# Performance work log

Hardware: AMD Instinct MI355X
Metric: run time of the kernel (lower is better)

The kernel has to match this reference:

```python
import jax, jax.numpy as jnp
import numpy as np

N, E, B = 20000, 160000, 1000
D_IN, HID, HEADS, CTX, EDIM, L = 7, 64, 4, 3, 5, 4


def _ln(x, g, b):
    mu = x.mean(-1, keepdims=True)
    v = ((x - mu) ** 2).mean(-1, keepdims=True)
    return (x - mu) / jnp.sqrt(v + 1e-5) * g + b


def _seg_softmax(a, seg, n):
    m = jax.ops.segment_max(a, seg, num_segments=n)
    e = jnp.exp(a - m[seg])
    s = jax.ops.segment_sum(e, seg, num_segments=n)
    return e / (s[seg] + 1e-16)


def _forward(x, edge_index, edge_attr, context, batch, role, side, formation, alignment, frame_t,
             emb_W, emb_b, role_tab, side_tab, ctx_W, ctx_b, form_tab, align_tab, temp_tab,
             gat_Wl, gat_bl, gat_Wr, gat_br, gat_We, gat_att, gat_bias,
             ln_g, ln_b, sp_W1, sp_b1, sp_W2, sp_b2, sp_Wg, sp_bg, fn_g, fn_b):
    src, dst = edge_index[0], edge_index[1]
    h = jax.nn.relu(x @ emb_W + emb_b)                      # [N, HID]
    h = h + role_tab[role]
    s_emb = side_tab[side]                                   # [N, HID//2], zero-padded to HID
    h = h + jnp.pad(s_emb, ((0, 0), (0, HID - HID // 2)))
    t_idx = jnp.clip((frame_t[0] * 99).astype(jnp.int32), 0, 99)
    h = h + temp_tab[t_idx]
    c = jax.nn.relu(context @ ctx_W + ctx_b)                 # [B, HID]
    c = c + form_tab[formation] + align_tab[alignment]
    h = h + c[batch]
    # PyG GATv2Conv adds self-loops (fill_value='mean' for edge_attr)
    in_cnt = jax.ops.segment_sum(jnp.ones((E,), h.dtype), dst, num_segments=N)
    loop_attr = jax.ops.segment_sum(edge_attr, dst, num_segments=N) / jnp.maximum(in_cnt, 1.0)[:, None]
    srcA = jnp.concatenate([src, jnp.arange(N, dtype=src.dtype)])
    dstA = jnp.concatenate([dst, jnp.arange(N, dtype=dst.dtype)])
    eaA = jnp.concatenate([edge_attr, loop_attr], axis=0)    # [E+N, EDIM]
    EA = E + N
    for i in range(L):
        h_res = h
        xl = (h @ gat_Wl[i] + gat_bl[i]).reshape(N, HEADS, HID)
        xr = (h @ gat_Wr[i] + gat_br[i]).reshape(N, HEADS, HID)
        e = (eaA @ gat_We[i]).reshape(EA, HEADS, HID)
        msg = jax.nn.leaky_relu(xl[srcA] + xr[dstA] + e, 0.2)  # [EA, H, C]
        alpha = jnp.einsum('ehc,hc->eh', msg, gat_att[i])
        alpha = _seg_softmax(alpha, dstA, N)
        agg = jax.ops.segment_sum(xl[srcA] * alpha[:, :, None], dstA, num_segments=N)
        h = agg.mean(axis=1) + gat_bias[i]                   # concat=False -> mean over heads
        h = jax.nn.relu(h)                                   # dropout is identity in eval
        h = _ln(h + h_res, ln_g[i], ln_b[i])
    # Social pooling: gather -> MLP -> gate -> scatter-mean by src
    pair = jnp.concatenate([h[src], h[dst]], axis=-1)        # [E, 2*HID]
    inter = jax.nn.relu(pair @ sp_W1 + sp_b1) @ sp_W2 + sp_b2
    gated = inter * jax.nn.sigmoid(inter @ sp_Wg + sp_bg)
    cnt = jax.ops.segment_sum(jnp.ones((E,), h.dtype), src, num_segments=N)
    pooled = jax.ops.segment_sum(gated, src, num_segments=N) / jnp.maximum(cnt, 1.0)[:, None]
    h = _ln(h + pooled, fn_g, fn_b)
    return h


def setup_inputs():
    key = jax.random.key(0)
    ks = jax.random.split(key, 32)
    p = lambda k, shp: jax.random.normal(k, shp, jnp.float32) * 0.05
    return dict(
        x=jax.random.normal(ks[0], (N, D_IN), jnp.float32),
        edge_index=jax.random.randint(ks[1], (2, E), 0, N),
        edge_attr=jax.random.normal(ks[2], (E, EDIM), jnp.float32),
        context=jax.random.normal(ks[3], (B, CTX), jnp.float32),
        batch=jax.random.randint(ks[4], (N,), 0, B),
        role=jax.random.randint(ks[5], (N,), 0, 5),
        side=jax.random.randint(ks[6], (N,), 0, 3),
        formation=jax.random.randint(ks[7], (B,), 0, 8),
        alignment=jax.random.randint(ks[8], (B,), 0, 10),
        frame_t=jax.random.uniform(ks[9], (1,), jnp.float32),
        emb_W=p(ks[10], (D_IN, HID)), emb_b=p(ks[11], (HID,)),
        role_tab=p(ks[12], (5, HID)), side_tab=p(ks[13], (3, HID // 2)),
        ctx_W=p(ks[14], (CTX, HID)), ctx_b=p(ks[15], (HID,)),
        form_tab=p(ks[16], (8, HID)), align_tab=p(ks[17], (10, HID)),
        temp_tab=p(ks[18], (100, HID)),
        gat_Wl=p(ks[19], (L, HID, HEADS * HID)), gat_bl=p(ks[20], (L, HEADS * HID)),
        gat_Wr=p(ks[21], (L, HID, HEADS * HID)), gat_br=p(ks[22], (L, HEADS * HID)),
        gat_We=p(ks[23], (L, EDIM, HEADS * HID)),
        gat_att=p(ks[24], (L, HEADS, HID)), gat_bias=p(ks[25], (L, HID)),
        ln_g=jnp.ones((L, HID), jnp.float32), ln_b=jnp.zeros((L, HID), jnp.float32),
        sp_W1=p(ks[26], (2 * HID, HID)), sp_b1=p(ks[27], (HID,)),
        sp_W2=p(ks[28], (HID, HID)), sp_b2=p(ks[29], (HID,)),
        sp_Wg=p(ks[30], (HID, HID)), sp_bg=p(ks[31], (HID,)),
        fn_g=jnp.ones((HID,), jnp.float32), fn_b=jnp.zeros((HID,), jnp.float32),
    )


def reference(x, edge_index, edge_attr, context, batch, role, side, formation, alignment, frame_t,
              emb_W, emb_b, role_tab, side_tab, ctx_W, ctx_b, form_tab, align_tab, temp_tab,
              gat_Wl, gat_bl, gat_Wr, gat_br, gat_We, gat_att, gat_bias,
              ln_g, ln_b, sp_W1, sp_b1, sp_W2, sp_b2, sp_Wg, sp_bg, fn_g, fn_b):
    return _forward(x, edge_index, edge_attr, context, batch, role, side, formation, alignment, frame_t,
                    emb_W, emb_b, role_tab, side_tab, ctx_W, ctx_b, form_tab, align_tab, temp_tab,
                    gat_Wl, gat_bl, gat_Wr, gat_br, gat_We, gat_att, gat_bias,
                    ln_g, ln_b, sp_W1, sp_b1, sp_W2, sp_b2, sp_Wg, sp_bg, fn_g, fn_b)
```

## Files before the change

kernel.cpp:

```cpp
#include <hip/hip_runtime.h>
#include <math.h>

constexpr int N = 20000, E = 160000, Bb = 1000;
constexpr int DIN = 7, HID = 64, HEADS = 4, CTXD = 3, EDIM = 5, NL = 4;
constexpr int HH = HEADS * HID;

__device__ __forceinline__ float wredsum(float v) {
#pragma unroll
  for (int o = 32; o; o >>= 1) v += __shfl_xor(v, o, 64);
  return v;
}

__global__ void k_node_init(const float* __restrict__ x, const float* __restrict__ emb_W,
                            const float* __restrict__ emb_b, const int* __restrict__ role,
                            const float* __restrict__ role_tab, const int* __restrict__ side,
                            const float* __restrict__ side_tab, const float* __restrict__ frame_t,
                            const float* __restrict__ temp_tab, const int* __restrict__ batch,
                            const float* __restrict__ ctx, const float* __restrict__ ctx_W,
                            const float* __restrict__ ctx_b, const float* __restrict__ form_tab,
                            const float* __restrict__ align_tab, const int* __restrict__ form,
                            const int* __restrict__ alig, float* __restrict__ h) {
  int t = blockIdx.x * blockDim.x + threadIdx.x;
  if (t >= N * HID) return;
  int n = t >> 6, j = t & 63;
  float a = emb_b[j];
#pragma unroll
  for (int k = 0; k < DIN; ++k) a += x[n * DIN + k] * emb_W[k * HID + j];
  a = fmaxf(a, 0.f);
  a += role_tab[role[n] * HID + j];
  if (j < 32) a += side_tab[side[n] * 32 + j];
  int ti = (int)(frame_t[0] * 99.f);
  ti = ti < 0 ? 0 : (ti > 99 ? 99 : ti);
  a += temp_tab[ti * HID + j];
  int b = batch[n];
  float c = ctx_b[j];
#pragma unroll
  for (int k = 0; k < CTXD; ++k) c += ctx[b * CTXD + k] * ctx_W[k * HID + j];
  c = fmaxf(c, 0.f);
  c += form_tab[form[b] * HID + j] + align_tab[alig[b] * HID + j];
  h[t] = a + c;
}

__global__ void k_count(const int* __restrict__ ei, int* __restrict__ deg_dst,
                        int* __restrict__ deg_src) {
  int e = blockIdx.x * blockDim.x + threadIdx.x;
  if (e >= E) return;
  atomicAdd(&deg_src[ei[e]], 1);
  atomicAdd(&deg_dst[ei[E + e]], 1);
}

__global__ void k_fuse(const float* __restrict__ W2, const float* __restrict__ Wg,
                       const float* __restrict__ b2, const float* __restrict__ bg,
                       float* __restrict__ W2g, float* __restrict__ bg2) {
  int t = blockIdx.x * 256 + threadIdx.x;
  if (t < HID * HID) {
    int i = t >> 6, j = t & 63;
    float a = 0.f;
#pragma unroll
    for (int k = 0; k < HID; ++k) a += W2[i * HID + k] * Wg[k * HID + j];
    W2g[t] = a;
  }
  if (t < HID) {
    float a = bg[t];
#pragma unroll
    for (int k = 0; k < HID; ++k) a += b2[k] * Wg[k * HID + t];
    bg2[t] = a;
  }
}

__global__ void k_scan2(const int* __restrict__ degA, int* __restrict__ rowA,
                        int* __restrict__ curA, const int* __restrict__ degB,
                        int* __restrict__ rowB, int* __restrict__ curB, int n) {
  __shared__ int wsum[16];
  __shared__ int carry;
  int t = threadIdx.x, wid = t >> 6, lane = t & 63;
  for (int pass = 0; pass < 2; ++pass) {
    const int* deg = pass ? degB : degA;
    int* row = pass ? rowB : rowA;
    int* cur = pass ? curB : curA;
    if (t == 0) carry = 0;
    __syncthreads();
    for (int base = 0; base < n; base += 1024) {
      int v = (base + t < n) ? deg[base + t] : 0;
      int s = v;
#pragma unroll
      for (int off = 1; off < 64; off <<= 1) {
        int x = __shfl_up(s, off, 64);
        if (lane >= off) s += x;
      }
      if (lane == 63) wsum[wid] = s;
      __syncthreads();
      if (wid == 0) {
        int ws = (lane < 16) ? wsum[lane] : 0;
#pragma unroll
        for (int off = 1; off < 16; off <<= 1) {
          int x = __shfl_up(ws, off, 64);
          if (lane >= off) ws += x;
        }
        if (lane < 16) wsum[lane] = ws;
      }
      __syncthreads();
      int wexcl = (wid == 0) ? 0 : wsum[wid - 1];
      int r = carry + wexcl + (s - v);
      if (base + t < n) {
        row[base + t] = r;
        cur[base + t] = r;
      }
      __syncthreads();
      if (t == 0) carry += wsum[15];
      __syncthreads();
    }
  }
}

__global__ void k_scatter(const int* __restrict__ ei, int* __restrict__ cur_dst,
                          int* __restrict__ cur_src, int* __restrict__ eid_dst,
                          int* __restrict__ esrc_dst, int* __restrict__ esrc_srt,
                          int* __restrict__ edst_srt) {
  int e = blockIdx.x * blockDim.x + threadIdx.x;
  if (e >= E) return;
  int s = ei[e], d = ei[E + e];
  int ps = atomicAdd(&cur_src[s], 1);
  esrc_srt[ps] = s;
  edst_srt[ps] = d;
  int pd = atomicAdd(&cur_dst[d], 1);
  eid_dst[pd] = e;
  esrc_dst[pd] = s;
}

__global__ void k_loop_attr(const int* __restrict__ row_dst, const int* __restrict__ deg_dst,
                            const int* __restrict__ eid_dst, const float* __restrict__ ea,
                            float* __restrict__ la) {
  int n = blockIdx.x * blockDim.x + threadIdx.x;
  if (n >= N) return;
  int beg = row_dst[n], cnt = deg_dst[n];
  float s[EDIM] = {0.f, 0.f, 0.f, 0.f, 0.f};
  for (int j = 0; j < cnt; ++j) {
    int e = eid_dst[beg + j];
#pragma unroll
    for (int k = 0; k < EDIM; ++k) s[k] += ea[(size_t)e * EDIM + k];
  }
  float inv = 1.f / fmaxf((float)cnt, 1.f);
#pragma unroll
  for (int k = 0; k < EDIM; ++k) la[n * EDIM + k] = s[k] * inv;
}

__global__ __launch_bounds__(256) void k_xlxr(const float* __restrict__ h,
                                              const float* __restrict__ Wl,
                                              const float* __restrict__ bl,
                                              const float* __restrict__ Wr,
                                              const float* __restrict__ br,
                                              float* __restrict__ xl, float* __restrict__ xr) {
  constexpr int NB = 16;
  __shared__ float hs[NB][HID];
  int n0 = blockIdx.x * NB;
  for (int idx = threadIdx.x; idx < NB * HID; idx += 256) {
    int r = idx >> 6, c = idx & 63;
    hs[r][c] = h[(n0 + r) * HID + c];
  }
  __syncthreads();
  int t = threadIdx.x;
  float wl[HID], wr[HID];
#pragma unroll
  for (int k = 0; k < HID; ++k) {
    wl[k] = Wl[k * HH + t];
    wr[k] = Wr[k * HH + t];
  }
  float blv = bl[t], brv = br[t];
#pragma unroll 4
  for (int r = 0; r < NB; ++r) {
    float al = blv, ar = brv;
#pragma unroll
    for (int k = 0; k < HID; ++k) {
      float hv = hs[r][k];
      al += hv * wl[k];
      ar += hv * wr[k];
    }
    xl[(size_t)(n0 + r) * HH + t] = al;
    xr[(size_t)(n0 + r) * HH + t] = ar;
  }
}

__global__ __launch_bounds__(256) void k_gat(
    const float* __restrict__ xl, const float* __restrict__ xr, const float* __restrict__ ea,
    const float* __restrict__ la, const int* __restrict__ row_dst,
    const int* __restrict__ deg_dst, const int* __restrict__ eid_dst,
    const int* __restrict__ esrc_dst, const float* __restrict__ We,
    const float* __restrict__ att, const float* __restrict__ biasL,
    const float* __restrict__ lng, const float* __restrict__ lnb, float* __restrict__ h) {
  __shared__ float heads[HEADS][HID];
  int n = blockIdx.x;
  int w = threadIdx.x >> 6, lane = threadIdx.x & 63;
  int g = lane >> 4, q = lane & 15, c4 = q * 4;
  float4 xr4 = *(const float4*)(xr + (size_t)n * HH + w * HID + c4);
  float4 att4 = *(const float4*)(att + w * HID + c4);
  float4 we4[EDIM];
#pragma unroll
  for (int k = 0; k < EDIM; ++k) we4[k] = *(const float4*)(We + k * HH + w * HID + c4);
  int beg = row_dst[n], cnt = deg_dst[n];
  int tot = cnt + 1;
  float mg = -INFINITY, sg = 0.f;
  float ax = 0.f, ay = 0.f, az = 0.f, aw2 = 0.f;
  int srcn_p;
  const float* eap_p;
  if (g == 0 || g >= tot) {
    srcn_p = n;
    eap_p = la + (size_t)n * EDIM;
  } else {
    int pos = beg + g - 1;
    srcn_p = esrc_dst[pos];
    eap_p = ea + (size_t)eid_dst[pos] * EDIM;
  }
  for (int j = 0; j * 4 < tot; ++j) {
    int idx = j * 4 + g;
    int srcn = srcn_p;
    const float* eap = eap_p;
    int idx2 = idx + 4;
    if (idx2 >= tot) {
      srcn_p = n;
      eap_p = la + (size_t)n * EDIM;
    } else {
      int pos = beg + idx2 - 1;
      srcn_p = esrc_dst[pos];
      eap_p = ea + (size_t)eid_dst[pos] * EDIM;
    }
    if (idx < tot) {
      float4 ep;
      ep.x = ep.y = ep.z = ep.w = 0.f;
#pragma unroll
      for (int k = 0; k < EDIM; ++k) {
        float ev = eap[k];
        ep.x += ev * we4[k].x;
        ep.y += ev * we4[k].y;
        ep.z += ev * we4[k].z;
        ep.w += ev * we4[k].w;
      }
      float4 xl4 = *(const float4*)(xl + (size_t)srcn * HH + w * HID + c4);
      float v0 = xl4.x + xr4.x + ep.x;
      float v1 = xl4.y + xr4.y + ep.y;
      float v2 = xl4.z + xr4.z + ep.z;
      float v3 = xl4.w + xr4.w + ep.w;
      v0 = v0 > 0.f ? v0 : 0.2f * v0;
      v1 = v1 > 0.f ? v1 : 0.2f * v1;
      v2 = v2 > 0.f ? v2 : 0.2f * v2;
      v3 = v3 > 0.f ? v3 : 0.2f * v3;
      float dot = v0 * att4.x + v1 * att4.y + v2 * att4.z + v3 * att4.w;
#pragma unroll
      for (int o = 1; o < 16; o <<= 1) dot += __shfl_xor(dot, o, 64);
      float nm = fmaxf(mg, dot);
      float sc = __expf(mg - nm);
      float pp = __expf(dot - nm);
      sg = sg * sc + pp;
      ax = ax * sc + pp * xl4.x;
      ay = ay * sc + pp * xl4.y;
      az = az * sc + pp * xl4.z;
      aw2 = aw2 * sc + pp * xl4.w;
      mg = nm;
    }
  }
  float mm = fmaxf(mg, __shfl_xor(mg, 16, 64));
  mm = fmaxf(mm, __shfl_xor(mm, 32, 64));
  float scale = __expf(mg - mm);
  float st = sg * scale;
  st += __shfl_xor(st, 16, 64);
  st += __shfl_xor(st, 32, 64);
  ax *= scale; ax += __shfl_xor(ax, 16, 64); ax += __shfl_xor(ax, 32, 64);
  ay *= scale; ay += __shfl_xor(ay, 16, 64); ay += __shfl_xor(ay, 32, 64);
  az *= scale; az += __shfl_xor(az, 16, 64); az += __shfl_xor(az, 32, 64);
  aw2 *= scale; aw2 += __shfl_xor(aw2, 16, 64); aw2 += __shfl_xor(aw2, 32, 64);
  float inv = 1.f / (st + 1e-16f);
  if (g == 0) {
    heads[w][c4 + 0] = ax * inv;
    heads[w][c4 + 1] = ay * inv;
    heads[w][c4 + 2] = az * inv;
    heads[w][c4 + 3] = aw2 * inv;
  }
  __syncthreads();
  if (w == 0) {
    float hv = (heads[0][lane] + heads[1][lane] + heads[2][lane] + heads[3][lane]) * 0.25f +
               biasL[lane];
    hv = fmaxf(hv, 0.f);
    float v = hv + h[n * HID + lane];
    float mu = wredsum(v) * (1.f / 64.f);
    float d = v - mu;
    float var = wredsum(d * d) * (1.f / 64.f);
    h[n * HID + lane] = d * rsqrtf(var + 1e-5f) * lng[lane] + lnb[lane];
  }
}

__global__ __launch_bounds__(256) void k_uv(const float* __restrict__ h,
                                            const float* __restrict__ W1,
                                            const float* __restrict__ b1,
                                            float* __restrict__ u, float* __restrict__ v) {
  constexpr int NB = 16;
  __shared__ float hs[NB][HID];
  int n0 = blockIdx.x * NB;
  for (int idx = threadIdx.x; idx < NB * HID; idx += 256) {
    int r = idx >> 6, c = idx & 63;
    int n = n0 + r;
    hs[r][c] = (n < N) ? h[n * HID + c] : 0.f;
  }
  __syncthreads();
  int j = threadIdx.x & 63, q = threadIdx.x >> 6;
  float wa[HID], wb[HID];
#pragma unroll
  for (int k = 0; k < HID; ++k) {
    wa[k] = W1[k * HID + j];
    wb[k] = W1[(HID + k) * HID + j];
  }
  float b1v = b1[j];
  for (int r = q; r < NB; r += 4) {
    int n = n0 + r;
    if (n >= N) continue;
    float au = b1v, av = 0.f;
#pragma unroll
    for (int k = 0; k < HID; ++k) {
      float hv = hs[r][k];
      au += hv * wa[k];
      av += hv * wb[k];
    }
    u[(size_t)n * HID + j] = au;
    v[(size_t)n * HID + j] = av;
  }
}

__global__ __launch_bounds__(256) void k_edge(const float* __restrict__ u,
                                              const float* __restrict__ v,
                                              const int* __restrict__ esrc_srt,
                                              const int* __restrict__ edst_srt,
                                              const float* __restrict__ W2,
                                              const float* __restrict__ b2,
                                              const float* __restrict__ W2g,
                                              const float* __restrict__ bg2,
                                              float* __restrict__ gated) {
  __shared__ float T[4][32 * 68];
  int w = threadIdx.x >> 6, lane = threadIdx.x & 63;
  float* Tw = T[w];
  int p0 = blockIdx.x * 128 + w * 32;
  float w2c[HID], wgc[HID];
#pragma unroll
  for (int k = 0; k < HID; ++k) {
    w2c[k] = W2[k * HID + lane];
    wgc[k] = W2g[k * HID + lane];
  }
  float b2v = b2[lane], bgv = bg2[lane];
  int sv = esrc_srt[p0 + (lane & 31)];
  int dv = edst_srt[p0 + (lane & 31)];
  for (int i = 0; i < 32; ++i) {
    int si = __shfl(sv, i, 64), di = __shfl(dv, i, 64);
    Tw[i * 68 + lane] = fmaxf(u[(size_t)si * HID + lane] + v[(size_t)di * HID + lane], 0.f);
  }
  __syncthreads();
#pragma unroll 2
  for (int i = 0; i < 32; ++i) {
    float it0 = b2v, gt0 = bgv, it1 = 0.f, gt1 = 0.f;
#pragma unroll
    for (int k4 = 0; k4 < 16; ++k4) {
      float4 a = *(const float4*)&Tw[i * 68 + k4 * 4];
      it0 += a.x * w2c[k4 * 4 + 0];
      gt0 += a.x * wgc[k4 * 4 + 0];
      it1 += a.y * w2c[k4 * 4 + 1];
      gt1 += a.y * wgc[k4 * 4 + 1];
      it0 += a.z * w2c[k4 * 4 + 2];
      gt0 += a.z * wgc[k4 * 4 + 2];
      it1 += a.w * w2c[k4 * 4 + 3];
      gt1 += a.w * wgc[k4 * 4 + 3];
    }
    float it = it0 + it1, gt = gt0 + gt1;
    gated[(size_t)(p0 + i) * HID + lane] = it / (1.f + __expf(-gt));
  }
}

__global__ void k_pool(const float* __restrict__ h, const float* __restrict__ gated,
                       const int* __restrict__ row_src, const int* __restrict__ deg_src,
                       const float* __restrict__ g, const float* __restrict__ b,
                       float* __restrict__ out) {
  int n = blockIdx.x * 4 + (threadIdx.x >> 6);
  int lane = threadIdx.x & 63;
  if (n >= N) return;
  int beg = row_src[n], cnt = deg_src[n];
  float acc = 0.f;
  for (int i = 0; i < cnt; ++i) acc += gated[(size_t)(beg + i) * HID + lane];
  float v = h[n * HID + lane] + acc / fmaxf((float)cnt, 1.f);
  float mu = wredsum(v) * (1.f / 64.f);
  float d = v - mu;
  float var = wredsum(d * d) * (1.f / 64.f);
  out[n * HID + lane] = d * rsqrtf(var + 1e-5f) * g[lane] + b[lane];
}

extern "C" void kernel_launch(void* const* d_in, const int* in_sizes, int n_in, void* d_out,
                              int out_size, void* d_ws, size_t ws_size, hipStream_t stream) {
  const float* x = (const float*)d_in[0];
  const int* ei = (const int*)d_in[1];
  const float* eattr = (const float*)d_in[2];
  const float* ctx = (const float*)d_in[3];
  const int* batch = (const int*)d_in[4];
  const int* role = (const int*)d_in[5];
  const int* side = (const int*)d_in[6];
  const int* form = (const int*)d_in[7];
  const int* alig = (const int*)d_in[8];
  const float* frame_t = (const float*)d_in[9];
  const float* emb_W = (const float*)d_in[10];
  const float* emb_b = (const float*)d_in[11];
  const float* role_tab = (const float*)d_in[12];
  const float* side_tab = (const float*)d_in[13];
  const float* ctx_W = (const float*)d_in[14];
  const float* ctx_b = (const float*)d_in[15];
  const float* form_tab = (const float*)d_in[16];
  const float* align_tab = (const float*)d_in[17];
  const float* temp_tab = (const float*)d_in[18];
  const float* gat_Wl = (const float*)d_in[19];
  const float* gat_bl = (const float*)d_in[20];
  const float* gat_Wr = (const float*)d_in[21];
  const float* gat_br = (const float*)d_in[22];
  const float* gat_We = (const float*)d_in[23];
  const float* gat_att = (const float*)d_in[24];
  const float* gat_bias = (const float*)d_in[25];
  const float* ln_g = (const float*)d_in[26];
  const float* ln_b = (const float*)d_in[27];
  const float* sp_W1 = (const float*)d_in[28];
  const float* sp_b1 = (const float*)d_in[29];
  const float* sp_W2 = (const float*)d_in[30];
  const float* sp_b2 = (const float*)d_in[31];
  const float* sp_Wg = (const float*)d_in[32];
  const float* sp_bg = (const float*)d_in[33];
  const float* fn_g = (const float*)d_in[34];
  const float* fn_b = (const float*)d_in[35];
  float* out = (float*)d_out;

  char* wp = (char*)d_ws;
  auto alloc = [&](size_t bytes) {
    void* p = (void*)wp;
    wp += (bytes + 255) & ~(size_t)255;
    return p;
  };
  float* h = (float*)alloc((size_t)N * HID * 4);
  float* xl = (float*)alloc((size_t)N * HH * 4);
  float* xr = (float*)alloc((size_t)N * HH * 4);
  float* la = (float*)alloc((size_t)N * EDIM * 4);
  float* u = (float*)alloc((size_t)N * HID * 4);
  float* v = (float*)alloc((size_t)N * HID * 4);
  float* W2g = (float*)alloc((size_t)HID * HID * 4);
  float* bg2 = (float*)alloc((size_t)HID * 4);
  int* deg_dst = (int*)alloc((size_t)N * 4);
  int* deg_src = (int*)alloc((size_t)N * 4);
  int* row_dst = (int*)alloc((size_t)N * 4);
  int* row_src = (int*)alloc((size_t)N * 4);
  int* cur_dst = (int*)alloc((size_t)N * 4);
  int* cur_src = (int*)alloc((size_t)N * 4);
  int* eid_dst = (int*)alloc((size_t)E * 4);
  int* esrc_dst = (int*)alloc((size_t)E * 4);
  int* esrc_srt = (int*)alloc((size_t)E * 4);
  int* edst_srt = (int*)alloc((size_t)E * 4);
  float* gated = xl;

  hipMemsetAsync(deg_dst, 0, (size_t)N * 4, stream);
  hipMemsetAsync(deg_src, 0, (size_t)N * 4, stream);

  k_node_init<<<(N * HID + 255) / 256, 256, 0, stream>>>(
      x, emb_W, emb_b, role, role_tab, side, side_tab, frame_t, temp_tab, batch, ctx, ctx_W,
      ctx_b, form_tab, align_tab, form, alig, h);
  k_count<<<(E + 255) / 256, 256, 0, stream>>>(ei, deg_dst, deg_src);
  k_fuse<<<16, 256, 0, stream>>>(sp_W2, sp_Wg, sp_b2, sp_bg, W2g, bg2);
  k_scan2<<<1, 1024, 0, stream>>>(deg_dst, row_dst, cur_dst, deg_src, row_src, cur_src, N);
  k_scatter<<<(E + 255) / 256, 256, 0, stream>>>(ei, cur_dst, cur_src, eid_dst, esrc_dst,
                                                 esrc_srt, edst_srt);
  k_loop_attr<<<(N + 255) / 256, 256, 0, stream>>>(row_dst, deg_dst, eid_dst, eattr, la);

  for (int i = 0; i < NL; ++i) {
    k_xlxr<<<N / 16, 256, 0, stream>>>(h, gat_Wl + (size_t)i * HID * HH, gat_bl + i * HH,
                                       gat_Wr + (size_t)i * HID * HH, gat_br + i * HH, xl, xr);
    k_gat<<<N, 256, 0, stream>>>(xl, xr, eattr, la, row_dst, deg_dst, eid_dst, esrc_dst,
                                 gat_We + (size_t)i * EDIM * HH, gat_att + i * HH,
                                 gat_bias + i * HID, ln_g + i * HID, ln_b + i * HID, h);
  }

  k_uv<<<(N + 15) / 16, 256, 0, stream>>>(h, sp_W1, sp_b1, u, v);
  k_edge<<<E / 128, 256, 0, stream>>>(u, v, esrc_srt, edst_srt, sp_W2, sp_b2, W2g, bg2, gated);
  k_pool<<<(N + 3) / 4, 256, 0, stream>>>(h, gated, row_src, deg_src, fn_g, fn_b, out);
}
```

Measured before the change: 640.0 us.

## Parallelize CSR degree scan across blocks and vectorize xl/xr dot products

Replaces the single-block 1024-thread serial-chunk prefix scan over node degrees with a three-kernel multi-block scan: per-block sums, a single-wave scan of the block totals, then a per-block apply. The goal is to remove the long serialized loop of one block walking about 20 chunks per array. Separately, the xl/xr projection kernel now reads shared-memory h values as float4 and splits each accumulation across two partial sums to shorten the dependent FMA chains. The cost is two extra kernel launches and a small extra buffer.

```diff
diff --git a/kernel.cpp b/kernel.cpp
--- a/kernel.cpp
+++ b/kernel.cpp
@@ -4,8 +4,15 @@
 constexpr int N = 20000, E = 160000, Bb = 1000;
 constexpr int DIN = 7, HID = 64, HEADS = 4, CTXD = 3, EDIM = 5, NL = 4;
 constexpr int HH = HEADS * HID;
+constexpr int SNB = (N + 255) / 256;
 
 __device__ __forceinline__ float wredsum(float v) {
+#pragma unroll
+  for (int o = 32; o; o >>= 1) v += __shfl_xor(v, o, 64);
+  return v;
+}
+
+__device__ __forceinline__ int wredsumi(int v) {
 #pragma unroll
   for (int o = 32; o; o >>= 1) v += __shfl_xor(v, o, 64);
   return v;
@@ -68,48 +75,78 @@
   }
 }
 
-__global__ void k_scan2(const int* __restrict__ degA, int* __restrict__ rowA,
-                        int* __restrict__ curA, const int* __restrict__ degB,
-                        int* __restrict__ rowB, int* __restrict__ curB, int n) {
-  __shared__ int wsum[16];
-  __shared__ int carry;
-  int t = threadIdx.x, wid = t >> 6, lane = t & 63;
-  for (int pass = 0; pass < 2; ++pass) {
-    const int* deg = pass ? degB : degA;
-    int* row = pass ? rowB : rowA;
-    int* cur = pass ? curB : curA;
-    if (t == 0) carry = 0;
-    __syncthreads();
-    for (int base = 0; base < n; base += 1024) {
-      int v = (base + t < n) ? deg[base + t] : 0;
+__global__ __launch_bounds__(256) void k_bsum(const int* __restrict__ dA,
+                                              const int* __restrict__ dB,
+                                              int* __restrict__ bsA, int* __restrict__ bsB) {
+  __shared__ int sA[4], sB[4];
+  int blk = blockIdx.x, t = threadIdx.x;
+  int wid = t >> 6, lane = t & 63;
+  int i = blk * 256 + t;
+  int vA = (i < N) ? dA[i] : 0;
+  int vB = (i < N) ? dB[i] : 0;
+  int rA = wredsumi(vA), rB = wredsumi(vB);
+  if (lane == 0) {
+    sA[wid] = rA;
+    sB[wid] = rB;
+  }
+  __syncthreads();
+  if (t == 0) {
+    bsA[blk] = sA[0] + sA[1] + sA[2] + sA[3];
+    bsB[blk] = sB[0] + sB[1] + sB[2] + sB[3];
+  }
+}
+
+__global__ __launch_bounds__(64) void k_bscan(int* __restrict__ bsA, int* __restrict__ bsB,
+                                              int nb) {
+  int lane = threadIdx.x;
+  for (int arr = 0; arr < 2; ++arr) {
+    int* bs = arr ? bsB : bsA;
+    int carry = 0;
+    for (int base = 0; base < nb; base += 64) {
+      int idx = base + lane;
+      int v = (idx < nb) ? bs[idx] : 0;
       int s = v;
 #pragma unroll
       for (int off = 1; off < 64; off <<= 1) {
         int x = __shfl_up(s, off, 64);
         if (lane >= off) s += x;
       }
-      if (lane == 63) wsum[wid] = s;
-      __syncthreads();
-      if (wid == 0) {
-        int ws = (lane < 16) ? wsum[lane] : 0;
-#pragma unroll
-        for (int off = 1; off < 16; off <<= 1) {
-          int x = __shfl_up(ws, off, 64);
-          if (lane >= off) ws += x;
-        }
-        if (lane < 16) wsum[lane] = ws;
-      }
-      __syncthreads();
-      int wexcl = (wid == 0) ? 0 : wsum[wid - 1];
-      int r = carry + wexcl + (s - v);
-      if (base + t < n) {
-        row[base + t] = r;
-        cur[base + t] = r;
-      }
-      __syncthreads();
-      if (t == 0) carry += wsum[15];
-      __syncthreads();
-    }
+      if (idx < nb) bs[idx] = carry + s - v;
+      carry += __shfl(s, 63, 64);
+    }
+  }
+}
+
+__global__ __launch_bounds__(256) void k_scan_apply(
+    const int* __restrict__ dA, const int* __restrict__ dB, const int* __restrict__ bsA,
+    const int* __restrict__ bsB, int* __restrict__ rowA, int* __restrict__ curA,
+    int* __restrict__ rowB, int* __restrict__ curB) {
+  __shared__ int ws[4];
+  int blk = blockIdx.x, t = threadIdx.x;
+  int wid = t >> 6, lane = t & 63;
+  int i = blk * 256 + t;
+  for (int arr = 0; arr < 2; ++arr) {
+    const int* deg = arr ? dB : dA;
+    const int* bs = arr ? bsB : bsA;
+    int* row = arr ? rowB : rowA;
+    int* cur = arr ? curB : curA;
+    int v = (i < N) ? deg[i] : 0;
+    int s = v;
+#pragma unroll
+    for (int off = 1; off < 64; off <<= 1) {
+      int x = __shfl_up(s, off, 64);
+      if (lane >= off) s += x;
+    }
+    if (lane == 63) ws[wid] = s;
+    __syncthreads();
+    int wexcl = 0;
+    for (int k = 0; k < wid; ++k) wexcl += ws[k];
+    int r = bs[blk] + wexcl + s - v;
+    if (i < N) {
+      row[i] = r;
+      cur[i] = r;
+    }
+    __syncthreads();
   }
 }
 
@@ -169,15 +206,21 @@
   float blv = bl[t], brv = br[t];
 #pragma unroll 4
   for (int r = 0; r < NB; ++r) {
-    float al = blv, ar = brv;
-#pragma unroll
-    for (int k = 0; k < HID; ++k) {
-      float hv = hs[r][k];
-      al += hv * wl[k];
-      ar += hv * wr[k];
-    }
-    xl[(size_t)(n0 + r) * HH + t] = al;
-    xr[(size_t)(n0 + r) * HH + t] = ar;
+    float al0 = blv, al1 = 0.f, ar0 = brv, ar1 = 0.f;
+#pragma unroll
+    for (int k4 = 0; k4 < 16; ++k4) {
+      float4 a = *(const float4*)&hs[r][k4 * 4];
+      al0 += a.x * wl[k4 * 4 + 0];
+      ar0 += a.x * wr[k4 * 4 + 0];
+      al1 += a.y * wl[k4 * 4 + 1];
+      ar1 += a.y * wr[k4 * 4 + 1];
+      al0 += a.z * wl[k4 * 4 + 2];
+      ar0 += a.z * wr[k4 * 4 + 2];
+      al1 += a.w * wl[k4 * 4 + 3];
+      ar1 += a.w * wr[k4 * 4 + 3];
+    }
+    xl[(size_t)(n0 + r) * HH + t] = al0 + al1;
+    xr[(size_t)(n0 + r) * HH + t] = ar0 + ar1;
   }
 }
 
@@ -452,6 +495,8 @@
   int* esrc_dst = (int*)alloc((size_t)E * 4);
   int* esrc_srt = (int*)alloc((size_t)E * 4);
   int* edst_srt = (int*)alloc((size_t)E * 4);
+  int* bsA = (int*)alloc((size_t)SNB * 4);
+  int* bsB = (int*)alloc((size_t)SNB * 4);
   float* gated = xl;
 
   hipMemsetAsync(deg_dst, 0, (size_t)N * 4, stream);
@@ -462,7 +507,10 @@
       ctx_b, form_tab, align_tab, form, alig, h);
   k_count<<<(E + 255) / 256, 256, 0, stream>>>(ei, deg_dst, deg_src);
   k_fuse<<<16, 256, 0, stream>>>(sp_W2, sp_Wg, sp_b2, sp_bg, W2g, bg2);
-  k_scan2<<<1, 1024, 0, stream>>>(deg_dst, row_dst, cur_dst, deg_src, row_src, cur_src, N);
+  k_bsum<<<SNB, 256, 0, stream>>>(deg_dst, deg_src, bsA, bsB);
+  k_bscan<<<1, 64, 0, stream>>>(bsA, bsB, SNB);
+  k_scan_apply<<<SNB, 256, 0, stream>>>(deg_dst, deg_src, bsA, bsB, row_dst, cur_dst, row_src,
+                                        cur_src);
   k_scatter<<<(E + 255) / 256, 256, 0, stream>>>(ei, cur_dst, cur_src, eid_dst, esrc_dst,
                                                  esrc_srt, edst_srt);
   k_loop_attr<<<(N + 255) / 256, 256, 0, stream>>>(row_dst, deg_dst, eid_dst, eattr, la);
```

Result: slower. 724.0 us (+13.1%).
